# Optimization experiments

Hardware: AMD Instinct MI355X
Metric: run time of the kernel (lower is better)

Reference implementation:

```python
import jax, jax.numpy as jnp
import numpy as np

SIGMA_E, SIGMA_I, K_E, K_I = 0.6, 1.2, 0.8, 1.0
PM_STEPS, DT, BETA = 4, 0.15, 1.0
EPS = 1e-4


def setup_inputs() -> dict:
    key = jax.random.key(0)
    ks = jax.random.split(key, 12)
    B, d_in, d_lat, ch, d_out, n_c = 4096, 784, 8, 32, 10, 16
    inp = {
        "x": jax.random.normal(ks[0], (B, d_in), dtype=jnp.float32),
        "W1": jax.random.normal(ks[1], (d_in, 128), dtype=jnp.float32) * 0.03,
        "b1": jnp.zeros((128,), jnp.float32),
        "W2": jax.random.normal(ks[2], (128, d_lat), dtype=jnp.float32) * 0.08,
        "b2": jnp.zeros((d_lat,), jnp.float32),
        "centers": jax.random.normal(ks[3], (n_c, d_lat), dtype=jnp.float32) * 0.7,
        "mus": jnp.ones((n_c,), jnp.float32) * 0.5,
        "Wp": jax.random.normal(ks[4], (d_lat, ch), dtype=jnp.float32) * 0.3,
        "bp": jnp.zeros((ch,), jnp.float32),
        "Wr": jax.random.normal(ks[5], (ch, d_out), dtype=jnp.float32) * 0.15,
        "br": jnp.zeros((d_out,), jnp.float32),
        "T": 5,
    }
    return inp


def grad_ln_n(z, centers, mus):
    # z: [B,d], centers: [C,d], mus: [C]
    rvec = z[:, None, :] - centers[None, :, :]          # [B,C,d]
    r = jnp.sqrt(jnp.sum(rvec * rvec, axis=-1) + EPS)   # [B,C]
    n = 1.0 + jnp.sum(mus[None, :] / r, axis=1)          # [B]
    g = -jnp.sum((mus[None, :] / (r ** 3))[:, :, None] * rvec, axis=1)  # [B,d]
    return g / n[:, None]


def pm_field(z, centers, mus):
    for _ in range(PM_STEPS):
        z = jnp.clip(z + DT * BETA * grad_ln_n(z, centers, mus), -3.0, 3.0)
    return z


def lateral_kernel(z):
    # squared pairwise distances via the norm trick (avoids [B,B,d])
    sq = jnp.sum(z * z, axis=1)
    dist2 = jnp.maximum(sq[:, None] + sq[None, :] - 2.0 * (z @ z.T), 0.0)
    K = K_E * jnp.exp(-dist2 / (2.0 * SIGMA_E ** 2)) - K_I * jnp.exp(-dist2 / (2.0 * SIGMA_I ** 2))
    return jax.lax.stop_gradient(K)  # torch.no_grad in original


def reference(x, W1, b1, W2, b2, centers, mus, Wp, bp, Wr, br, T):
    B = x.shape[0]
    z = jnp.tanh(x.reshape(B, -1) @ W1 + b1) @ W2 + b2   # encoder
    h = jnp.zeros((B, Wr.shape[0]), x.dtype)
    for _ in range(T):
        z = pm_field(z, centers, mus)
        h = 0.9 * h + 0.1 * jnp.tanh(z @ Wp + bp)
        h = h + 0.05 * (lateral_kernel(z) @ h)
        y = h @ Wr + br
    return y
```

## Files before the change

kernel.cpp:

```cpp
#include <hip/hip_runtime.h>
#include <math.h>

#define NB    4096
#define DIN   784
#define DH    128
#define DL    8
#define NC    16
#define NCH   32
#define DO    10
#define TSTEPS 5

#define KH_ROWS   128
#define KH_JSLICE 128
#define KH_P      (NB / KH_JSLICE)
#define ENC_G     7

typedef float v2f __attribute__((ext_vector_type(2)));


__global__ __launch_bounds__(256) void enc1_kernel(const float* __restrict__ x,
    const float* __restrict__ W1, double* __restrict__ P)
{
    __shared__ float xsT[56][36];
    __shared__ float wss[56][132];
    const int tid = threadIdx.x;
    const int m0 = blockIdx.x * 32;
    const int kbeg = blockIdx.y * 112;
    const int cg = tid & 31, rg = tid >> 5;
    const int c0 = cg << 2, r0 = rg << 2;
    double acc[4][4] = {};
    for (int it = 0; it < 2; ++it) {
        const int k0 = kbeg + it * 56;
        __syncthreads();
        for (int l = tid; l < 448; l += 256) {
            int row = l / 14, f = l % 14;
            float4 v = *(const float4*)(x + (m0 + row) * DIN + k0 + f * 4);
            int kk = f * 4;
            xsT[kk][row] = v.x; xsT[kk + 1][row] = v.y;
            xsT[kk + 2][row] = v.z; xsT[kk + 3][row] = v.w;
        }
        for (int l = tid; l < 56 * 32; l += 256) {
            int kk = l >> 5, c = (l & 31) << 2;
            *(float4*)&wss[kk][c] = *(const float4*)(W1 + (k0 + kk) * DH + c);
        }
        __syncthreads();
#pragma unroll 4
        for (int kk = 0; kk < 56; ++kk) {
            const float4 xv = *(const float4*)&xsT[kk][r0];
            const float4 wv = *(const float4*)&wss[kk][c0];
            const double x0 = (double)xv.x, x1 = (double)xv.y;
            const double x2 = (double)xv.z, x3 = (double)xv.w;
            const double w0 = (double)wv.x, w1 = (double)wv.y;
            const double w2v = (double)wv.z, w3 = (double)wv.w;
            acc[0][0] += x0 * w0; acc[0][1] += x0 * w1; acc[0][2] += x0 * w2v; acc[0][3] += x0 * w3;
            acc[1][0] += x1 * w0; acc[1][1] += x1 * w1; acc[1][2] += x1 * w2v; acc[1][3] += x1 * w3;
            acc[2][0] += x2 * w0; acc[2][1] += x2 * w1; acc[2][2] += x2 * w2v; acc[2][3] += x2 * w3;
            acc[3][0] += x3 * w0; acc[3][1] += x3 * w1; acc[3][2] += x3 * w2v; acc[3][3] += x3 * w3;
        }
    }
    double* Pr = P + (size_t)blockIdx.y * (NB * DH);
#pragma unroll
    for (int i = 0; i < 4; ++i) {
        double* dst = Pr + (m0 + r0 + i) * DH + c0;
        *(double2*)dst       = make_double2(acc[i][0], acc[i][1]);
        *(double2*)(dst + 2) = make_double2(acc[i][2], acc[i][3]);
    }
}

__global__ __launch_bounds__(256) void enc2_kernel(const double* __restrict__ P,
    const float* __restrict__ b1, const float* __restrict__ W2,
    const float* __restrict__ b2, double* __restrict__ zbuf)
{
    __shared__ double As[16][132];
    __shared__ double W2d[DH * DL];
    const int tid = threadIdx.x;
    const int m0 = blockIdx.x * 16;
    for (int l = tid; l < DH * DL; l += 256) W2d[l] = (double)W2[l];
    for (int l = tid; l < 16 * 128; l += 256) {
        int row = l >> 7, k = l & 127;
        double v = (double)b1[k];
#pragma unroll
        for (int s = 0; s < ENC_G; ++s)
            v += P[(size_t)s * NB * DH + (m0 + row) * DH + k];
        As[row][k] = tanh(v);
    }
    __syncthreads();
    const int row = tid >> 4, d = (tid >> 1) & 7, half = tid & 1;
    double a = 0.0;
#pragma unroll 8
    for (int i = 0; i < 64; ++i) {
        const int k = half + (i << 1);
        a += As[row][k] * W2d[k * 8 + d];
    }
    a += __shfl_xor(a, 1);
    if (half == 0) zbuf[(m0 + row) * DL + d] = a + (double)b2[d];
}

__global__ __launch_bounds__(256) void enc_fused_kernel(const float* __restrict__ x,
    const float* __restrict__ W1, const float* __restrict__ b1,
    const float* __restrict__ W2, const float* __restrict__ b2,
    double* __restrict__ zbuf)
{
    __shared__ float  xsT[56][9];
    __shared__ float  wss[56][128];
    __shared__ double Asd[8][131];
    __shared__ double W2d[DH * DL];
    const int tid = threadIdx.x;
    const int m0 = blockIdx.x * 8;
    const int cg = tid & 31, rg = tid >> 5;
    const int c0 = cg << 2;
    for (int l = tid; l < DH * DL; l += 256) W2d[l] = (double)W2[l];
    double acc[4] = {};
    for (int it = 0; it < 14; ++it) {
        const int k0 = it * 56;
        __syncthreads();
        if (tid < 112) {
            int row = tid / 14, f = tid % 14;
            float4 v = *(const float4*)(x + (m0 + row) * DIN + k0 + f * 4);
            int kk = f * 4;
            xsT[kk][row] = v.x; xsT[kk + 1][row] = v.y;
            xsT[kk + 2][row] = v.z; xsT[kk + 3][row] = v.w;
        }
        for (int l = tid; l < 56 * 32; l += 256) {
            int kk = l >> 5, c = (l & 31) << 2;
            *(float4*)&wss[kk][c] = *(const float4*)(W1 + (k0 + kk) * DH + c);
        }
        __syncthreads();
#pragma unroll 8
        for (int kk = 0; kk < 56; ++kk) {
            const double xv = (double)xsT[kk][rg];
            const float4 wv = *(const float4*)&wss[kk][c0];
            acc[0] += xv * (double)wv.x;
            acc[1] += xv * (double)wv.y;
            acc[2] += xv * (double)wv.z;
            acc[3] += xv * (double)wv.w;
        }
    }
    __syncthreads();
#pragma unroll
    for (int j = 0; j < 4; ++j)
        Asd[rg][c0 + j] = tanh(acc[j] + (double)b1[c0 + j]);
    __syncthreads();
    {
        const int row = tid >> 5, d = (tid >> 2) & 7, kq = tid & 3;
        double a = 0.0;
#pragma unroll 8
        for (int i = 0; i < 32; ++i) {
            const int k = kq + (i << 2);
            a += Asd[row][k] * W2d[k * 8 + d];
        }
        a += __shfl_xor(a, 1);
        a += __shfl_xor(a, 2);
        if (kq == 0) zbuf[(m0 + row) * DL + d] = a + (double)b2[d];
    }
}

__global__ __launch_bounds__(64) void pmh_kernel(double* __restrict__ zbuf,
    const float* __restrict__ centers, const float* __restrict__ mus,
    const float* __restrict__ Wp, const float* __restrict__ bp,
    double* __restrict__ hB, float* __restrict__ zf, float* __restrict__ sqf,
    float* __restrict__ hAf, const float* __restrict__ part, int first)
{
    const int tid = threadIdx.x;
    const int lane = tid & 15;
    const int s = tid >> 4;
    const int i = blockIdx.x * 4 + s;
    double cz[8];
#pragma unroll
    for (int d = 0; d < 8; ++d) cz[d] = (double)centers[lane * DL + d];
    const double mu = (double)mus[lane];
    double z[8];
#pragma unroll
    for (int p = 0; p < 4; ++p) {
        double2 v = *(const double2*)(zbuf + i * DL + p * 2);
        z[p * 2] = v.x; z[p * 2 + 1] = v.y;
    }
#pragma unroll
    for (int st = 0; st < 4; ++st) {
        double rv[8];
        double ss = 1e-4;
#pragma unroll
        for (int d = 0; d < 8; ++d) { rv[d] = z[d] - cz[d]; ss += rv[d] * rv[d]; }
        double rinv = rsqrt(ss);
        double mr = mu * rinv;
        double n = mr;
        double mr3 = mr * (rinv * rinv);
        double g[8];
#pragma unroll
        for (int d = 0; d < 8; ++d) g[d] = -mr3 * rv[d];
#pragma unroll
        for (int m = 1; m < 16; m <<= 1) {
            n += __shfl_xor(n, m);
#pragma unroll
            for (int d = 0; d < 8; ++d) g[d] += __shfl_xor(g[d], m);
        }
        double sc = 0.15 / (1.0 + n);
#pragma unroll
        for (int d = 0; d < 8; ++d) z[d] = fmin(3.0, fmax(-3.0, z[d] + sc * g[d]));
    }
    if (lane == 0) {
        double sq = 0.0;
#pragma unroll
        for (int d = 0; d < 8; ++d) sq += z[d] * z[d];
        sqf[i] = (float)sq;
#pragma unroll
        for (int p = 0; p < 4; ++p)
            *(double2*)(zbuf + i * DL + p * 2) = make_double2(z[p * 2], z[p * 2 + 1]);
        float4 a = make_float4((float)z[0], (float)z[1], (float)z[2], (float)z[3]);
        float4 b = make_float4((float)z[4], (float)z[5], (float)z[6], (float)z[7]);
        *(float4*)(zf + i * DL)     = a;
        *(float4*)(zf + i * DL + 4) = b;
    }
#pragma unroll
    for (int cc = 0; cc < 2; ++cc) {
        const int c = lane + cc * 16;
        double a = (double)bp[c];
#pragma unroll
        for (int d = 0; d < 8; ++d) a += z[d] * (double)Wp[d * NCH + c];
        double ph = (double)tanhf((float)a);
        double prev = 0.0;
        if (!first) {
            prev = hB[i * NCH + c];
            if (part) {
                double sp = 0.0;
#pragma unroll
                for (int p = 0; p < KH_P; ++p)
                    sp += (double)part[(size_t)p * (NB * NCH) + i * NCH + c];
                prev += 0.05 * sp;
            }
        }
        double hv = 0.9 * prev + 0.1 * ph;
        hAf[i * NCH + c] = (float)hv;
        hB[i * NCH + c] = hv;
    }
}

#define SM_Z   0
#define SM_SQ  1024
#define SM_H   1152
#define SM_ALL 5248
__global__ __launch_bounds__(256) void kh_kernel(const float* __restrict__ zf,
    const float* __restrict__ sqf, const float* __restrict__ hAf,
    double* __restrict__ hB, float* __restrict__ part)
{
    __shared__ float smem[SM_ALL];
    const int tid = threadIdx.x;
    const int wave = tid >> 6, lane = tid & 63;
    const int row0 = blockIdx.x * KH_ROWS + lane;
    const int j0 = blockIdx.y * KH_JSLICE;
    float zr0[8], zr1[8];
    {
        float4 a = *(const float4*)(zf + row0 * 8);
        float4 b = *(const float4*)(zf + row0 * 8 + 4);
        zr0[0] = a.x; zr0[1] = a.y; zr0[2] = a.z; zr0[3] = a.w;
        zr0[4] = b.x; zr0[5] = b.y; zr0[6] = b.z; zr0[7] = b.w;
        float4 c = *(const float4*)(zf + (row0 + 64) * 8);
        float4 d = *(const float4*)(zf + (row0 + 64) * 8 + 4);
        zr1[0] = c.x; zr1[1] = c.y; zr1[2] = c.z; zr1[3] = c.w;
        zr1[4] = d.x; zr1[5] = d.y; zr1[6] = d.z; zr1[7] = d.w;
    }
    const float sq0 = sqf[row0], sq1 = sqf[row0 + 64];
    const float invI = 1.0f / 2.88f;
    {
        int jj = tid >> 1, p = (tid & 1) << 2;
        *(float4*)&smem[SM_Z + jj * 8 + p] = *(const float4*)(zf + (j0 + jj) * 8 + p);
    }
    if (tid < KH_JSLICE) smem[SM_SQ + tid] = sqf[j0 + tid];
    for (int l = tid; l < KH_JSLICE * 8; l += 256) {
        int jh = l >> 3, p = (l & 7) << 2;
        *(float4*)&smem[SM_H + jh * 32 + p] = *(const float4*)(hAf + (j0 + jh) * NCH + p);
    }
    __syncthreads();
    v2f a0[16], a1[16];
#pragma unroll
    for (int k = 0; k < 16; ++k) { a0[k] = (v2f)(0.f); a1[k] = (v2f)(0.f); }
    const int jjbeg = wave * 32;
#pragma unroll 2
    for (int q = 0; q < 32; ++q) {
        const int jj = jjbeg + q;
        const float4 a = *(const float4*)&smem[SM_Z + jj * 8];
        const float4 b = *(const float4*)&smem[SM_Z + jj * 8 + 4];
        const float sqj = smem[SM_SQ + jj];
        float dot0 = zr0[0] * a.x + zr0[1] * a.y + zr0[2] * a.z + zr0[3] * a.w
                   + zr0[4] * b.x + zr0[5] * b.y + zr0[6] * b.z + zr0[7] * b.w;
        float dot1 = zr1[0] * a.x + zr1[1] * a.y + zr1[2] * a.z + zr1[3] * a.w
                   + zr1[4] * b.x + zr1[5] * b.y + zr1[6] * b.z + zr1[7] * b.w;
        float d20 = fmaxf(sq0 + sqj - 2.0f * dot0, 0.0f);
        float d21 = fmaxf(sq1 + sqj - 2.0f * dot1, 0.0f);
        float e0 = __expf(-d20 * invI), e1 = __expf(-d21 * invI);
        float t0 = e0 * e0, t1 = e1 * e1;
        float K0 = 0.8f * (t0 * t0) - e0;
        float K1 = 0.8f * (t1 * t1) - e1;
        const v2f K0v = {K0, K0}, K1v = {K1, K1};
        const v2f* hrow = (const v2f*)&smem[SM_H + jj * 32];
#pragma unroll
        for (int k = 0; k < 16; k += 2) {
            const v2f h0 = hrow[k], h1 = hrow[k + 1];
            a0[k]     += K0v * h0; a0[k + 1] += K0v * h1;
            a1[k]     += K1v * h0; a1[k + 1] += K1v * h1;
        }
    }
    float* acc0 = (float*)a0;
    float* acc1 = (float*)a1;
    __syncthreads();
    if (wave == 1) {
#pragma unroll
        for (int c = 0; c < 32; ++c) { smem[lane * 33 + c] = acc0[c]; smem[(lane + 64) * 33 + c] = acc1[c]; }
    }
    __syncthreads();
    if (wave == 0) {
#pragma unroll
        for (int c = 0; c < 32; ++c) { acc0[c] += smem[lane * 33 + c]; acc1[c] += smem[(lane + 64) * 33 + c]; }
    }
    __syncthreads();
    if (wave == 3) {
#pragma unroll
        for (int c = 0; c < 32; ++c) { smem[lane * 33 + c] = acc0[c]; smem[(lane + 64) * 33 + c] = acc1[c]; }
    }
    __syncthreads();
    if (wave == 2) {
#pragma unroll
        for (int c = 0; c < 32; ++c) { acc0[c] += smem[lane * 33 + c]; acc1[c] += smem[(lane + 64) * 33 + c]; }
    }
    __syncthreads();
    if (wave == 2) {
#pragma unroll
        for (int c = 0; c < 32; ++c) { smem[lane * 33 + c] = acc0[c]; smem[(lane + 64) * 33 + c] = acc1[c]; }
    }
    __syncthreads();
    if (wave == 0) {
#pragma unroll
        for (int c = 0; c < 32; ++c) { acc0[c] += smem[lane * 33 + c]; acc1[c] += smem[(lane + 64) * 33 + c]; }
        if (part) {
            float* p0 = part + (size_t)blockIdx.y * (NB * NCH) + row0 * NCH;
            float* p1 = p0 + 64 * NCH;
#pragma unroll
            for (int c = 0; c < 32; c += 4) {
                *(float4*)(p0 + c) = make_float4(acc0[c], acc0[c + 1], acc0[c + 2], acc0[c + 3]);
                *(float4*)(p1 + c) = make_float4(acc1[c], acc1[c + 1], acc1[c + 2], acc1[c + 3]);
            }
        } else {
#pragma unroll
            for (int c = 0; c < 32; ++c) {
                atomicAdd(&hB[row0 * NCH + c], 0.05 * (double)acc0[c]);
                atomicAdd(&hB[(row0 + 64) * NCH + c], 0.05 * (double)acc1[c]);
            }
        }
    }
}

__global__ __launch_bounds__(256) void y_kernel(const double* __restrict__ h,
    const float* __restrict__ part, const float* __restrict__ Wr,
    const float* __restrict__ br, float* __restrict__ y)
{
    __shared__ double hsy[16][33];
    __shared__ double wrs[NCH * DO];
    __shared__ double brs[DO];
    const int tid = threadIdx.x;
    const int rb = blockIdx.x * 16;
    for (int l = tid; l < 16 * 32; l += 256) {
        int row = l >> 5, k = l & 31;
        const int gi = (rb + row) * NCH + k;
        double v = h[gi];
        if (part) {
            double sp = 0.0;
#pragma unroll
            for (int p = 0; p < KH_P; ++p) sp += (double)part[(size_t)p * (NB * NCH) + gi];
            v += 0.05 * sp;
        }
        hsy[row][k] = v;
    }
    for (int l = tid; l < NCH * DO; l += 256) wrs[l] = (double)Wr[l];
    if (tid < DO) brs[tid] = (double)br[tid];
    __syncthreads();
    const int row = tid >> 4, col = tid & 15;
    if (col < DO) {
        double a = brs[col];
#pragma unroll
        for (int k = 0; k < NCH; ++k) a += hsy[row][k] * wrs[k * DO + col];
        y[(rb + row) * DO + col] = (float)a;
    }
}

extern "C" void kernel_launch(void* const* d_in, const int* in_sizes, int n_in,
                              void* d_out, int out_size, void* d_ws, size_t ws_size,
                              hipStream_t stream)
{
    const float* x   = (const float*)d_in[0];
    const float* W1  = (const float*)d_in[1];
    const float* b1  = (const float*)d_in[2];
    const float* W2  = (const float*)d_in[3];
    const float* b2  = (const float*)d_in[4];
    const float* cen = (const float*)d_in[5];
    const float* mus = (const float*)d_in[6];
    const float* Wp  = (const float*)d_in[7];
    const float* bp  = (const float*)d_in[8];
    const float* Wr  = (const float*)d_in[9];
    const float* br  = (const float*)d_in[10];

    float* y = (float*)d_out;
    double* zbuf = (double*)d_ws;
    double* hB   = zbuf + NB * DL;
    float*  zf   = (float*)(hB + NB * NCH);
    float*  sqf  = zf + NB * DL;
    float*  hAf  = sqf + NB;
    float*  part = hAf + NB * NCH;
    double* Penc = (double*)(part + (size_t)KH_P * NB * NCH);

    const size_t need_part = (size_t)(NB * DL + NB * NCH) * 8
                           + (size_t)(NB * DL + NB + NB * NCH + KH_P * NB * NCH) * 4;
    const size_t need_full = need_part + (size_t)ENC_G * NB * DH * 8;
    float* pp = (ws_size >= need_part) ? part : (float*)nullptr;

    if (ws_size >= need_full) {
        enc1_kernel<<<dim3(NB / 32, ENC_G), 256, 0, stream>>>(x, W1, Penc);
        enc2_kernel<<<NB / 16, 256, 0, stream>>>(Penc, b1, W2, b2, zbuf);
    } else {
        enc_fused_kernel<<<NB / 8, 256, 0, stream>>>(x, W1, b1, W2, b2, zbuf);
    }
    for (int t = 0; t < TSTEPS; ++t) {
        pmh_kernel<<<NB / 4, 64, 0, stream>>>(zbuf, cen, mus, Wp, bp, hB,
                                              zf, sqf, hAf, pp, t == 0 ? 1 : 0);
        kh_kernel<<<dim3(NB / KH_ROWS, KH_P), 256, 0, stream>>>(zf, sqf, hAf, hB, pp);
    }
    y_kernel<<<NB / 16, 256, 0, stream>>>(hB, pp, Wr, br, y);
}
```

Measured before the change: 328.9 us.

## Split PM dims across lane pairs and parallelize kh cross-wave reduction

```diff
diff --git a/kernel.cpp b/kernel.cpp
--- a/kernel.cpp
+++ b/kernel.cpp
@@ -162,61 +162,74 @@
     float* __restrict__ hAf, const float* __restrict__ part, int first)
 {
     const int tid = threadIdx.x;
-    const int lane = tid & 15;
-    const int s = tid >> 4;
-    const int i = blockIdx.x * 4 + s;
-    double cz[8];
-#pragma unroll
-    for (int d = 0; d < 8; ++d) cz[d] = (double)centers[lane * DL + d];
-    const double mu = (double)mus[lane];
-    double z[8];
-#pragma unroll
-    for (int p = 0; p < 4; ++p) {
-        double2 v = *(const double2*)(zbuf + i * DL + p * 2);
-        z[p * 2] = v.x; z[p * 2 + 1] = v.y;
+    const int l32 = tid & 31;
+    const int slot = tid >> 5;
+    const int i = blockIdx.x * 2 + slot;
+    const int c16 = l32 >> 1;
+    const int hf = l32 & 1;
+    const int db = hf << 2;
+    double cz[4];
+#pragma unroll
+    for (int k = 0; k < 4; ++k) cz[k] = (double)centers[c16 * DL + db + k];
+    const double mu = (double)mus[c16];
+    double z4[4];
+    {
+        double2 v = *(const double2*)(zbuf + i * DL + db);
+        double2 w = *(const double2*)(zbuf + i * DL + db + 2);
+        z4[0] = v.x; z4[1] = v.y; z4[2] = w.x; z4[3] = w.y;
     }
 #pragma unroll
     for (int st = 0; st < 4; ++st) {
-        double rv[8];
-        double ss = 1e-4;
-#pragma unroll
-        for (int d = 0; d < 8; ++d) { rv[d] = z[d] - cz[d]; ss += rv[d] * rv[d]; }
+        double rv[4];
+        double ssp = 0.0;
+#pragma unroll
+        for (int k = 0; k < 4; ++k) { rv[k] = z4[k] - cz[k]; ssp += rv[k] * rv[k]; }
+        double ss = 1e-4 + ssp + __shfl_xor(ssp, 1);
         double rinv = rsqrt(ss);
         double mr = mu * rinv;
-        double n = mr;
+        double np = hf ? 0.0 : mr;
         double mr3 = mr * (rinv * rinv);
-        double g[8];
-#pragma unroll
-        for (int d = 0; d < 8; ++d) g[d] = -mr3 * rv[d];
-#pragma unroll
-        for (int m = 1; m < 16; m <<= 1) {
-            n += __shfl_xor(n, m);
-#pragma unroll
-            for (int d = 0; d < 8; ++d) g[d] += __shfl_xor(g[d], m);
-        }
-        double sc = 0.15 / (1.0 + n);
-#pragma unroll
-        for (int d = 0; d < 8; ++d) z[d] = fmin(3.0, fmax(-3.0, z[d] + sc * g[d]));
-    }
-    if (lane == 0) {
+        double g[4];
+#pragma unroll
+        for (int k = 0; k < 4; ++k) g[k] = -mr3 * rv[k];
+#pragma unroll
+        for (int m = 2; m <= 16; m <<= 1) {
+            np += __shfl_xor(np, m);
+#pragma unroll
+            for (int k = 0; k < 4; ++k) g[k] += __shfl_xor(g[k], m);
+        }
+        np += __shfl_xor(np, 1);
+        double sc = 0.15 / (1.0 + np);
+#pragma unroll
+        for (int k = 0; k < 4; ++k) z4[k] = fmin(3.0, fmax(-3.0, z4[k] + sc * g[k]));
+    }
+    double zo[4];
+#pragma unroll
+    for (int k = 0; k < 4; ++k) zo[k] = __shfl_xor(z4[k], 1);
+    double zfull[8];
+#pragma unroll
+    for (int k = 0; k < 4; ++k) {
+        zfull[k]     = hf ? zo[k] : z4[k];
+        zfull[4 + k] = hf ? z4[k] : zo[k];
+    }
+    if (l32 == 0) {
         double sq = 0.0;
 #pragma unroll
-        for (int d = 0; d < 8; ++d) sq += z[d] * z[d];
+        for (int d = 0; d < 8; ++d) sq += zfull[d] * zfull[d];
         sqf[i] = (float)sq;
 #pragma unroll
         for (int p = 0; p < 4; ++p)
-            *(double2*)(zbuf + i * DL + p * 2) = make_double2(z[p * 2], z[p * 2 + 1]);
-        float4 a = make_float4((float)z[0], (float)z[1], (float)z[2], (float)z[3]);
-        float4 b = make_float4((float)z[4], (float)z[5], (float)z[6], (float)z[7]);
+            *(double2*)(zbuf + i * DL + p * 2) = make_double2(zfull[p * 2], zfull[p * 2 + 1]);
+        float4 a = make_float4((float)zfull[0], (float)zfull[1], (float)zfull[2], (float)zfull[3]);
+        float4 b = make_float4((float)zfull[4], (float)zfull[5], (float)zfull[6], (float)zfull[7]);
         *(float4*)(zf + i * DL)     = a;
         *(float4*)(zf + i * DL + 4) = b;
     }
-#pragma unroll
-    for (int cc = 0; cc < 2; ++cc) {
-        const int c = lane + cc * 16;
+    {
+        const int c = l32;
         double a = (double)bp[c];
 #pragma unroll
-        for (int d = 0; d < 8; ++d) a += z[d] * (double)Wp[d * NCH + c];
+        for (int d = 0; d < 8; ++d) a += zfull[d] * (double)Wp[d * NCH + c];
         double ph = (double)tanhf((float)a);
         double prev = 0.0;
         if (!first) {
@@ -238,7 +251,8 @@
 #define SM_Z   0
 #define SM_SQ  1024
 #define SM_H   1152
-#define SM_ALL 5248
+#define SM_R2  4224
+#define SM_ALL 8448
 __global__ __launch_bounds__(256) void kh_kernel(const float* __restrict__ zf,
     const float* __restrict__ sqf, const float* __restrict__ hAf,
     double* __restrict__ hB, float* __restrict__ part)
@@ -307,20 +321,18 @@
 #pragma unroll
         for (int c = 0; c < 32; ++c) { smem[lane * 33 + c] = acc0[c]; smem[(lane + 64) * 33 + c] = acc1[c]; }
     }
+    if (wave == 3) {
+#pragma unroll
+        for (int c = 0; c < 32; ++c) { smem[SM_R2 + lane * 33 + c] = acc0[c]; smem[SM_R2 + (lane + 64) * 33 + c] = acc1[c]; }
+    }
     __syncthreads();
     if (wave == 0) {
 #pragma unroll
         for (int c = 0; c < 32; ++c) { acc0[c] += smem[lane * 33 + c]; acc1[c] += smem[(lane + 64) * 33 + c]; }
     }
-    __syncthreads();
-    if (wave == 3) {
-#pragma unroll
-        for (int c = 0; c < 32; ++c) { smem[lane * 33 + c] = acc0[c]; smem[(lane + 64) * 33 + c] = acc1[c]; }
-    }
-    __syncthreads();
     if (wave == 2) {
 #pragma unroll
-        for (int c = 0; c < 32; ++c) { acc0[c] += smem[lane * 33 + c]; acc1[c] += smem[(lane + 64) * 33 + c]; }
+        for (int c = 0; c < 32; ++c) { acc0[c] += smem[SM_R2 + lane * 33 + c]; acc1[c] += smem[SM_R2 + (lane + 64) * 33 + c]; }
     }
     __syncthreads();
     if (wave == 2) {
@@ -419,7 +431,7 @@
         enc_fused_kernel<<<NB / 8, 256, 0, stream>>>(x, W1, b1, W2, b2, zbuf);
     }
     for (int t = 0; t < TSTEPS; ++t) {
-        pmh_kernel<<<NB / 4, 64, 0, stream>>>(zbuf, cen, mus, Wp, bp, hB,
+        pmh_kernel<<<NB / 2, 64, 0, stream>>>(zbuf, cen, mus, Wp, bp, hB,
                                               zf, sqf, hAf, pp, t == 0 ? 1 : 0);
         kh_kernel<<<dim3(NB / KH_ROWS, KH_P), 256, 0, stream>>>(zf, sqf, hAf, hB, pp);
     }
```

Result: no change. 325.1 us (-1.2%).
